# Kernel tuning notes

Measured on AMD Instinct MI355X. Metric: run time of the kernel, lower is better.

## Reference

```python
import jax, jax.numpy as jnp
import numpy as np
from functools import partial

IMG = 800
ANCHOR_SIZES = (32.0, 64.0, 128.0, 256.0, 512.0)
RATIOS = (0.5, 1.0, 2.0)
PRE_NMS = 1000
POST_NMS = 1000
NMS_TH = 0.7
MIN_SIZE = 1e-3
POOL = 7
SRATIO = 2  # roi_align sampling_ratio
SCALES = (0.25, 0.125, 0.0625, 0.03125)
BBOX_CLIP = float(np.log(1000.0 / 16.0))


def _cell_anchors(size):
    r = jnp.asarray(RATIOS, jnp.float32)
    hr = jnp.sqrt(r)
    wr = 1.0 / hr
    ws = size * wr
    hs = size * hr
    return jnp.round(jnp.stack([-ws / 2, -hs / 2, ws / 2, hs / 2], axis=1))  # [A,4]


def _grid_anchors(gh, gw, sh, sw, cell):
    sx = jnp.arange(gw, dtype=jnp.float32) * sw
    sy = jnp.arange(gh, dtype=jnp.float32) * sh
    yy, xx = jnp.meshgrid(sy, sx, indexing='ij')
    shifts = jnp.stack([xx, yy, xx, yy], axis=-1).reshape(-1, 4)
    # order: H-major, W, then A anchors per cell (matches torchvision)
    return (shifts[:, None, :] + cell[None, :, :]).reshape(-1, 4)


def _flatten_level(obj, dl):
    # permute_and_flatten: [B,A,H,W] -> [B,H*W*A], [B,4A,H,W] -> [B,H*W*A,4]
    B, A, H, W = obj.shape
    o = obj.transpose(0, 2, 3, 1).reshape(B, -1)
    d = dl.reshape(B, A, 4, H, W).transpose(0, 3, 4, 1, 2).reshape(B, -1, 4)
    return o, d


def _decode(deltas, anchors):
    # BoxCoder.decode with weights (1,1,1,1)
    w = anchors[:, 2] - anchors[:, 0]
    h = anchors[:, 3] - anchors[:, 1]
    cx = anchors[:, 0] + 0.5 * w
    cy = anchors[:, 1] + 0.5 * h
    dx, dy = deltas[..., 0], deltas[..., 1]
    dw = jnp.minimum(deltas[..., 2], BBOX_CLIP)
    dh = jnp.minimum(deltas[..., 3], BBOX_CLIP)
    pcx = dx * w + cx
    pcy = dy * h + cy
    pw = jnp.exp(dw) * w
    ph = jnp.exp(dh) * h
    return jnp.stack([pcx - 0.5 * pw, pcy - 0.5 * ph, pcx + 0.5 * pw, pcy + 0.5 * ph], axis=-1)


def _iou_one(box, boxes):
    a1 = (box[2] - box[0]) * (box[3] - box[1])
    a2 = (boxes[:, 2] - boxes[:, 0]) * (boxes[:, 3] - boxes[:, 1])
    lt = jnp.maximum(box[:2], boxes[:, :2])
    rb = jnp.minimum(box[2:], boxes[:, 2:])
    wh = jnp.clip(rb - lt, 0.0)
    inter = wh[:, 0] * wh[:, 1]
    return inter / (a1 + a2 - inter)


def _nms(boxes, scores, k):
    # greedy NMS, fixed k iterations (jit-friendly)
    def step(s, _):
        i = jnp.argmax(s)
        sup = _iou_one(boxes[i], boxes) > NMS_TH
        s = jnp.where(sup, -jnp.inf, s).at[i].set(-jnp.inf)
        return s, i
    _, idx = jax.lax.scan(step, scores, None, length=k)
    return idx


def _roi_align(feat, rois, scale):
    # feat [C,H,W], rois [R,4] in image coords -> [R,C,POOL,POOL]; aligned=False semantics
    C, H, W = feat.shape
    R = rois.shape[0]
    x1, y1 = rois[:, 0] * scale, rois[:, 1] * scale
    x2, y2 = rois[:, 2] * scale, rois[:, 3] * scale
    rw = jnp.maximum(x2 - x1, 1.0)
    rh = jnp.maximum(y2 - y1, 1.0)
    S = POOL * SRATIO
    t = (jnp.arange(S, dtype=jnp.float32) + 0.5) / S
    y = jnp.broadcast_to((y1[:, None] + rh[:, None] * t)[:, :, None], (R, S, S))
    x = jnp.broadcast_to((x1[:, None] + rw[:, None] * t)[:, None, :], (R, S, S))
    mask = (y >= -1.0) & (y <= H) & (x >= -1.0) & (x <= W)
    yc = jnp.clip(y, 0.0, H - 1.0)
    xc = jnp.clip(x, 0.0, W - 1.0)
    y0 = jnp.floor(yc).astype(jnp.int32)
    x0 = jnp.floor(xc).astype(jnp.int32)
    y1i = jnp.minimum(y0 + 1, H - 1)
    x1i = jnp.minimum(x0 + 1, W - 1)
    ly = yc - y0
    lx = xc - x0
    v00 = feat[:, y0, x0]
    v01 = feat[:, y0, x1i]
    v10 = feat[:, y1i, x0]
    v11 = feat[:, y1i, x1i]  # [C,R,S,S]
    val = ((1 - ly) * (1 - lx) * v00 + (1 - ly) * lx * v01 + ly * (1 - lx) * v10 + ly * lx * v11) * mask
    pooled = val.reshape(C, R, POOL, SRATIO, POOL, SRATIO).mean(axis=(3, 5))
    return pooled.transpose(1, 0, 2, 3)


def _forward(image_tensors, feats, objs, dls):
    B = image_tensors.shape[0]
    grids = [o.shape[-2:] for o in objs]
    anchors = jnp.concatenate([
        _grid_anchors(gh, gw, float(IMG // gh), float(IMG // gw), _cell_anchors(s))
        for (gh, gw), s in zip(grids, ANCHOR_SIZES)], axis=0)
    flat = [_flatten_level(o, d) for o, d in zip(objs, dls)]
    # RPN detaches both objectness and deltas before proposal filtering
    obj = jax.lax.stop_gradient(jnp.concatenate([f[0] for f in flat], axis=1))   # [B,N]
    dl = jax.lax.stop_gradient(jnp.concatenate([f[1] for f in flat], axis=1))    # [B,N,4]
    proposals = _decode(dl, anchors)                                             # [B,N,4]
    npl = [3 * gh * gw for gh, gw in grids]
    offs = np.concatenate([[0], np.cumsum(npl)])
    idx_parts, lvl_parts = [], []
    for l, n in enumerate(npl):
        k = min(PRE_NMS, n)
        _, ix = jax.lax.top_k(obj[:, offs[l]:offs[l + 1]], k)
        idx_parts.append(ix + offs[l])
        lvl_parts.append(jnp.full((k,), l, jnp.float32))
    idx = jnp.concatenate(idx_parts, axis=1)   # [B,K]
    lvl = jnp.concatenate(lvl_parts)           # [K]
    boxes = jnp.take_along_axis(proposals, idx[..., None], axis=1)
    scores = jax.nn.sigmoid(jnp.take_along_axis(obj, idx, axis=1))
    boxes = jnp.clip(boxes, 0.0, float(IMG))   # clip_boxes_to_image (square image)
    ws = boxes[..., 2] - boxes[..., 0]
    hs = boxes[..., 3] - boxes[..., 1]
    valid = (ws >= MIN_SIZE) & (hs >= MIN_SIZE)  # remove_small_boxes via score masking
    scores = jnp.where(valid, scores, -jnp.inf)
    # batched_nms: offset boxes per level so NMS is independent across levels
    off_boxes = boxes + (lvl * (IMG + 1.0))[None, :, None]
    keep = jax.vmap(lambda b, s: _nms(b, s, POST_NMS))(off_boxes, scores)  # [B,POST]
    props = jnp.take_along_axis(boxes, keep[..., None], axis=1)            # [B,POST,4]
    # MultiScaleRoIAlign level mapping (k0=4, canonical 224)
    area = (props[..., 2] - props[..., 0]) * (props[..., 3] - props[..., 1])
    li = jnp.clip(jnp.floor(4.0 + jnp.log2(jnp.sqrt(area) / 224.0 + 1e-6)), 2.0, 5.0).astype(jnp.int32) - 2
    R = props.shape[1]
    C = feats[0].shape[1]
    box_feats = jnp.zeros((B, R, C, POOL, POOL), feats[0].dtype)
    for l, (f, sc) in enumerate(zip(feats, SCALES)):
        pooled = jax.vmap(partial(_roi_align, scale=sc))(f, props)  # [B,R,C,7,7]
        box_feats = box_feats + pooled * (li == l)[..., None, None, None]
    return props, box_feats.reshape(B * R, C, POOL, POOL)


def setup_inputs() -> dict:
    key = jax.random.key(0)
    ks = jax.random.split(key, 16)
    B, C = 2, 256
    grids = [(200, 200), (100, 100), (50, 50), (25, 25), (13, 13)]
    d = {}
    d['image_tensors'] = jax.random.normal(ks[0], (B, 3, IMG, IMG), jnp.float32)
    for i in range(4):
        gh, gw = grids[i]
        d[f'features_{i}'] = jax.random.normal(ks[1 + i], (B, C, gh, gw), jnp.float32)
    for i in range(5):
        gh, gw = grids[i]
        d[f'objectness_{i}'] = jax.random.normal(ks[5 + i], (B, 3, gh, gw), jnp.float32)
        d[f'pred_bbox_deltas_{i}'] = jax.random.normal(ks[10 + i], (B, 12, gh, gw), jnp.float32)
    return d


def reference(image_tensors, features_0, features_1, features_2, features_3,
              objectness_0, objectness_1, objectness_2, objectness_3, objectness_4,
              pred_bbox_deltas_0, pred_bbox_deltas_1, pred_bbox_deltas_2,
              pred_bbox_deltas_3, pred_bbox_deltas_4):
    feats = [features_0, features_1, features_2, features_3]
    objs = [objectness_0, objectness_1, objectness_2, objectness_3, objectness_4]
    dls = [pred_bbox_deltas_0, pred_bbox_deltas_1, pred_bbox_deltas_2,
           pred_bbox_deltas_3, pred_bbox_deltas_4]
    return _forward(image_tensors, feats, objs, dls)
```

## Files before the change

kernel.cpp:

```cpp
#include <hip/hip_runtime.h>
#include <math.h>

typedef unsigned int u32;
typedef unsigned long long u64;

#define N_ALL 159882
#define NC 4507
#define MROW 72
#define NEGINF_KEY 0x007FFFFFu
#define IMGF 800.0f
#define BBOX_CLIP_F 4.135166556742356f

#define NHWC_L1 10240000u
#define NHWC_L2 12800000u
#define NHWC_L3 13440000u
#define NHWC_BS 13600000u

__constant__ int   c_offs[5]  = {0,120000,150000,157500,159375};
__constant__ int   c_gw[5]    = {200,100,50,25,13};
__constant__ float c_stride[5]= {4.f,8.f,16.f,32.f,61.f};
__constant__ float c_size[5]  = {32.f,64.f,128.f,256.f,512.f};
__constant__ int   c_koff[5]  = {0,1000,2000,3000,4000};
__constant__ int   c_k[5]     = {1000,1000,1000,1000,507};
__constant__ float c_ratio[3] = {0.5f,1.f,2.f};

struct PtrArgs { const float* obj[5]; const float* dl[5]; };

__device__ __forceinline__ u32 fkey32f(float x){
  u32 u = __float_as_uint(x);
  return (u & 0x80000000u) ? ~u : (u | 0x80000000u);
}
__device__ __forceinline__ int level_of(int g){
  return (g >= 159375) ? 4 : (g >= 157500) ? 3 : (g >= 150000) ? 2 : (g >= 120000) ? 1 : 0;
}
__device__ __forceinline__ u64 readlane64(u64 v, int l){
  u32 lo = (u32)v, hi = (u32)(v >> 32);
  u32 a = (u32)__builtin_amdgcn_readlane((int)lo, l);
  u32 b = (u32)__builtin_amdgcn_readlane((int)hi, l);
  return ((u64)b << 32) | (u64)a;
}

__global__ void k_decode(PtrArgs pa, int B, float* boxes_all, u32* key_all, u32* fkey_all){
#pragma clang fp contract(off)
  int idx = blockIdx.x*blockDim.x + threadIdx.x;
  int total = B*N_ALL;
  if (idx >= total) return;
  int b = idx / N_ALL;
  int g = idx - b*N_ALL;
  int l = level_of(g);
  int n = g - c_offs[l];
  int a = n % 3;
  int pos = n / 3;
  int gw = c_gw[l];
  int wx = pos % gw;
  int hy = pos / gw;
  int plane = gw*gw;
  const float* obj = pa.obj[l];
  const float* dl  = pa.dl[l];
  float logit = obj[(size_t)(b*3 + a)*plane + hy*gw + wx];
  size_t dbase = (size_t)(b*12 + a*4)*plane + (size_t)hy*gw + wx;
  float d0 = dl[dbase];
  float d1 = dl[dbase + (size_t)plane];
  float d2 = dl[dbase + (size_t)2*plane];
  float d3 = dl[dbase + (size_t)3*plane];
  float ratio = c_ratio[a];
  float hr = sqrtf(ratio);
  float wr = 1.0f/hr;
  float wsz = c_size[l]*wr;
  float hsz = c_size[l]*hr;
  float ca0 = rintf(-0.5f*wsz), ca1 = rintf(-0.5f*hsz);
  float ca2 = rintf( 0.5f*wsz), ca3 = rintf( 0.5f*hsz);
  float st = c_stride[l];
  float shx = (float)wx*st, shy = (float)hy*st;
  float ax1 = shx+ca0, ay1 = shy+ca1, ax2 = shx+ca2, ay2 = shy+ca3;
  float w = ax2-ax1, h = ay2-ay1;
  float cx = ax1 + 0.5f*w, cy = ay1 + 0.5f*h;
  float dw = fminf(d2, BBOX_CLIP_F), dh = fminf(d3, BBOX_CLIP_F);
  float pcx = d0*w + cx, pcy = d1*h + cy;
  float pw = expf(dw)*w, ph = expf(dh)*h;
  float x1 = pcx - 0.5f*pw, y1 = pcy - 0.5f*ph;
  float x2 = pcx + 0.5f*pw, y2 = pcy + 0.5f*ph;
  x1 = fminf(fmaxf(x1,0.f),IMGF); y1 = fminf(fmaxf(y1,0.f),IMGF);
  x2 = fminf(fmaxf(x2,0.f),IMGF); y2 = fminf(fmaxf(y2,0.f),IMGF);
  bool valid = ((x2-x1) >= 0.001f) && ((y2-y1) >= 0.001f);
  ((float4*)boxes_all)[idx] = make_float4(x1,y1,x2,y2);
  key_all[idx] = fkey32f(logit);
  float sgf = 1.0f/(1.0f + expf(-logit));
  fkey_all[idx] = valid ? fkey32f(sgf) : NEGINF_KEY;
}

__global__ __launch_bounds__(1024) void k_topk(const u32* key_all, u32* cand_g, int B){
  int blk = blockIdx.x;
  int b = blk / 5, l = blk - b*5;
  int g0 = c_offs[l];
  int N  = ((l==4)?N_ALL:c_offs[l+1]) - g0;
  int k  = c_k[l];
  const u32* keys = key_all + (size_t)b*N_ALL + g0;
  u32* out = cand_g + (size_t)b*NC + c_koff[l];
  __shared__ u32 hist[4096];
  __shared__ u64 buf[4096];
  __shared__ int s_bstar, s_chi, s_scnt, s_bcnt;
  int tid = threadIdx.x;
  for (int i=tid;i<4096;i+=1024) hist[i]=0;
  if (tid==0){ s_scnt=0; s_bcnt=0; }
  __syncthreads();
  for (int i=tid;i<N;i+=1024) atomicAdd(&hist[keys[i]>>20], 1u);
  __syncthreads();
  for (int s=1;s<4096;s<<=1){
    u32 v[4];
    for (int j=0;j<4;j++){ int i=tid+j*1024; v[j]=hist[i] + ((i+s<4096)?hist[i+s]:0); }
    __syncthreads();
    for (int j=0;j<4;j++){ int i=tid+j*1024; hist[i]=v[j]; }
    __syncthreads();
  }
  for (int j=0;j<4;j++){
    int i = tid + j*1024;
    u32 suf = hist[i];
    u32 nxt = (i+1<4096)?hist[i+1]:0u;
    if (suf >= (u32)k && nxt < (u32)k){ s_bstar = i; s_chi = (int)nxt; }
  }
  __syncthreads();
  int bstar = s_bstar, chi = s_chi;
  int r = k - chi;
  for (int i=tid;i<N;i+=1024){
    u32 kk = keys[i];
    int bin = (int)(kk>>20);
    if (bin > bstar){
      int slot = atomicAdd(&s_scnt,1);
      out[slot] = (u32)(g0 + i);
    } else if (bin == bstar){
      int slot = atomicAdd(&s_bcnt,1);
      if (slot < 4096) buf[slot] = ((u64)kk<<32) | (u32)(~(u32)(g0+i));
    }
  }
  __syncthreads();
  int m = s_bcnt; if (m > 4096) m = 4096;
  int P = 1; while (P < m) P <<= 1; if (P < 2) P = 2;
  for (int i=m+tid;i<P;i+=1024) buf[i]=0;
  __syncthreads();
  for (u32 ksz=2;ksz<=(u32)P;ksz<<=1){
    for (u32 j=ksz>>1;j>0;j>>=1){
      for (int i=tid;i<P;i+=1024){
        u32 ixj = (u32)i ^ j;
        if (ixj > (u32)i){
          u64 x = buf[i], y = buf[ixj];
          bool up = ((i & ksz) == 0);
          if (up ? (x < y) : (x > y)){ buf[i]=y; buf[ixj]=x; }
        }
      }
      __syncthreads();
    }
  }
  for (int t=tid; t<r && t<m; t+=1024) out[chi + t] = ~(u32)buf[t];
}

__global__ __launch_bounds__(1024) void k_rank(u32* cand_g, const u32* key_all, int B){
  int blk = blockIdx.x; int b = blk/5, l = blk - b*5;
  int k = c_k[l];
  u32* seg = cand_g + (size_t)b*NC + c_koff[l];
  __shared__ u64 sk[1024];
  int tid = threadIdx.x;
  u64 v = 0;
  if (tid < k){
    u32 g = seg[tid];
    v = ((u64)key_all[(size_t)b*N_ALL + g]<<32) | (u32)(~g);
  }
  sk[tid] = v;
  __syncthreads();
  for (u32 ksz=2;ksz<=1024;ksz<<=1){
    for (u32 j=ksz>>1;j>0;j>>=1){
      int i = tid;
      u32 ixj = (u32)i ^ j;
      if (ixj > (u32)i){
        u64 x = sk[i], y = sk[ixj];
        bool up = ((i & ksz) == 0);
        if (up ? (x < y) : (x > y)){ sk[i]=y; sk[ixj]=x; }
      }
      __syncthreads();
    }
  }
  if (tid < k) seg[tid] = ~(u32)sk[tid];
}

__device__ __forceinline__ void merge_elem(const u64* As, const u64* Bs, u64* dst,
                                           int m, int n, int k){
  int lo = k - n; if (lo < 0) lo = 0;
  int hi = (k < m) ? k : m;
  while (lo < hi){
    int mid = (lo + hi) >> 1;
    if (As[mid] > Bs[k-1-mid]) lo = mid + 1; else hi = mid;
  }
  int a = lo, bb = k - lo;
  u64 out;
  if (a < m && (bb >= n || As[a] > Bs[bb])) out = As[a]; else out = Bs[bb];
  dst[k] = out;
}

__global__ __launch_bounds__(1024) void k_sortcand(const u32* cand_g, const u32* fkey_all,
                                                   const float* boxes_all,
                                                   float* sorted_box, float* sorted_off,
                                                   u32* fcnt_ws, float* pos0box){
  __shared__ u64 sA[NC];
  __shared__ u64 sB[NC];
  __shared__ u32 wsum[16];
  __shared__ int s_f;
  int b = blockIdx.x, tid = threadIdx.x;
  int lane = tid & 63, wv = tid >> 6;
  if (tid == 0) s_f = 0;
  size_t cbase = (size_t)b*NC;
  size_t abase = (size_t)b*N_ALL;
  u64 below = lane ? (~0ull >> (64 - lane)) : 0ull;
  for (int l = 0; l < 5; ++l){
    int kl = c_k[l], ko = c_koff[l];
    bool act = tid < kl;
    u32 fk = 0; bool val = false;
    u32 i_g = (u32)(ko + tid);
    if (act){
      u32 g = cand_g[cbase + i_g];
      fk = fkey_all[abase + g];
      val = fk > NEGINF_KEY;
    }
    u64 bal = __ballot(act && val);
    int pv_w = __popcll(bal & below);
    if (lane == 0) wsum[wv] = (u32)__popcll(bal);
    __syncthreads();
    int pre = 0, Vl = 0;
    #pragma unroll
    for (int w2 = 0; w2 < 16; ++w2){
      int s = (int)wsum[w2];
      if (w2 < wv) pre += s;
      Vl += s;
    }
    if (tid == 0) s_f += Vl;
    if (act){
      int pv = pre + pv_w;
      int pos = val ? pv : (Vl + (tid - pv));
      sA[ko + pos] = ((u64)fk << 32) | (u32)(~i_g);
    }
    __syncthreads();
  }
  for (int k = tid; k < NC; k += 1024){
    if (k < 2000)       merge_elem(sA,        sA + 1000, sB,        1000, 1000, k);
    else if (k < 4000)  merge_elem(sA + 2000, sA + 3000, sB + 2000, 1000, 1000, k - 2000);
    else                sB[k] = sA[k];
  }
  __syncthreads();
  for (int k = tid; k < NC; k += 1024){
    if (k < 4000) merge_elem(sB, sB + 2000, sA, 2000, 2000, k);
    else          sA[k] = sB[k];
  }
  __syncthreads();
  for (int k = tid; k < NC; k += 1024){
    merge_elem(sA, sA + 4000, sB, 4000, 507, k);
  }
  __syncthreads();
  for (int i = tid; i < NC; i += 1024){
    u32 posc = ~(u32)sB[i];
    u32 g = cand_g[cbase + posc];
    int lvl = level_of((int)g);
    float4 bx = ((const float4*)boxes_all)[abase + g];
    ((float4*)sorted_box)[cbase + i] = bx;
    float off = 801.0f*(float)lvl;
    ((float4*)sorted_off)[cbase + i] = make_float4(bx.x+off, bx.y+off, bx.z+off, bx.w+off);
  }
  if (tid == 0){
    fcnt_ws[b] = (u32)s_f;
    u32 g0b = cand_g[cbase + 0];
    float4 bx = ((const float4*)boxes_all)[abase + g0b];
    ((float4*)pos0box)[b] = bx;
  }
}

__global__ void k_iou(const float* sorted_off, u64* M){
#pragma clang fp contract(off)
  int i = blockIdx.x, b = blockIdx.y, lane = threadIdx.x;
  const float4* boxes = ((const float4*)sorted_off) + (size_t)b*NC;
  float4 bi = boxes[i];
  float a1 = (bi.z-bi.x)*(bi.w-bi.y);
  u64* row = M + ((size_t)b*NC + i)*MROW;
  for (int w=0; w<71; w++){
    int j = w*64 + lane;
    bool sup = false;
    if (j < NC){
      float4 bj = boxes[j];
      float a2 = (bj.z-bj.x)*(bj.w-bj.y);
      float ltx = fmaxf(bi.x,bj.x), lty = fmaxf(bi.y,bj.y);
      float rbx = fminf(bi.z,bj.z), rby = fminf(bi.w,bj.w);
      float wx = fmaxf(rbx-ltx,0.f), wy = fmaxf(rby-lty,0.f);
      float inter = wx*wy;
      float iou = inter/(a1+a2-inter);
      sup = iou > 0.7f;
    }
    u64 word = __ballot(sup);
    if (lane==0) row[w] = word;
  }
}

#define GETQ2(q) { if (t2){ int jj=__builtin_ctzll(t2); t2&=t2-1; q = &buf[cb][jj*72]; } else q = zbuf; }
__global__ __launch_bounds__(256) void k_nms_tr(const float* sorted_box, const u64* M,
                      const u32* fcnt_ws, const float* pos0box, float* props, int B,
                      const float* f0, const float* f1, const float* f2, const float* f3,
                      float* nhwc, int doTr){
  __shared__ u64 buf[2][64*72];
  __shared__ u64 zbuf[72];
  __shared__ int ki[1000];
  __shared__ int s_kc, s_done;
  int bid = blockIdx.x;
  int tid = threadIdx.x;
  if (bid >= B){
    float (*t)[65] = reinterpret_cast<float(*)[65]>(&buf[0][0]);
    int id = bid - B;
    int b = id / 3328;
    int rem = id - b*3328;
    int P, W; const float* f; u32 loff;
    if (rem < 2500){ W=200; f=f0; loff=0u; }
    else if (rem < 3128){ W=100; f=f1; loff=NHWC_L1; rem -= 2500; }
    else if (rem < 3288){ W=50;  f=f2; loff=NHWC_L2; rem -= 3128; }
    else { W=25; f=f3; loff=NHWC_L3; rem -= 3288; }
    P = W*W;
    int ctile = rem & 3, ptile = rem >> 2;
    int c0 = ctile*64, p0 = ptile*64;
    const float* src = f + (size_t)b*256*P;
    float* dst = nhwc + (size_t)b*NHWC_BS + loff;
    int q   = tid & 15;
    int cl0 = tid >> 4;
    bool vec4ok = ((P & 3) == 0);
    int p = p0 + 4*q;
    float4 v[4];
    #pragma unroll
    for (int k = 0; k < 4; ++k){
      int cl = cl0 + 16*k;
      const float* s = src + (size_t)(c0+cl)*P + p;
      if (vec4ok && (p + 3 < P)){
        v[k] = *(const float4*)s;
      } else {
        v[k].x = (p   < P) ? s[0] : 0.f;
        v[k].y = (p+1 < P) ? s[1] : 0.f;
        v[k].z = (p+2 < P) ? s[2] : 0.f;
        v[k].w = (p+3 < P) ? s[3] : 0.f;
      }
    }
    #pragma unroll
    for (int k = 0; k < 4; ++k){
      int cl = cl0 + 16*k;
      t[cl][4*q+0] = v[k].x; t[cl][4*q+1] = v[k].y;
      t[cl][4*q+2] = v[k].z; t[cl][4*q+3] = v[k].w;
    }
    __syncthreads();
    #pragma unroll
    for (int k = 0; k < 4; ++k){
      int pl = cl0 + 16*k;
      int pp = p0 + pl;
      if (pp < P){
        float4 o = make_float4(t[4*q+0][pl], t[4*q+1][pl],
                               t[4*q+2][pl], t[4*q+3][pl]);
        *(float4*)(dst + (size_t)pp*256 + c0 + 4*q) = o;
      }
    }
    return;
  }
  int b = bid;
  int F = (int)fcnt_ws[b];
  const u64* Mb = M + (size_t)b*NC*MROW;
  int nch = (F + 63) >> 6;
  int lane = tid & 63, wv = tid >> 6;
  if (tid == 0){ s_kc = 0; s_done = (nch == 0) ? 1 : 0; }
  if (tid < 72) zbuf[tid] = 0ull;
  if (nch > 0){
    for (int e = tid; e < 64*72; e += 256){
      int rr = e / 72, wo = e - rr*72;
      int r2 = rr; if (r2 > NC-1) r2 = NC-1;
      buf[0][e] = Mb[(size_t)r2*MROW + wo];
    }
  }
  u64 rg[24];
  if (wv > 0 && nch > 1){
    #pragma unroll
    for (int k = 0; k < 24; ++k){
      int e = (tid - 64) + k*192;
      int rr = e/72, wo = e - rr*72;
      int r2 = 64 + rr; if (r2 > NC-1) r2 = NC-1;
      rg[k] = Mb[(size_t)r2*MROW + wo];
    }
  }
  __syncthreads();
  u64 sup0 = 0, sup1 = 0;
  int kc = 0;
  for (int c = 0; c < nch; ++c){
    int cb = c & 1;
    if (wv > 0){
      if (c + 1 < nch){
        #pragma unroll
        for (int k = 0; k < 24; ++k){
          int e = (tid - 64) + k*192;
          buf[cb^1][e] = rg[k];
        }
      }
      if (c + 2 < nch){
        int base2 = (c + 2) << 6;
        #pragma unroll
        for (int k = 0; k < 24; ++k){
          int e = (tid - 64) + k*192;
          int rr = e/72, wo = e - rr*72;
          int r2 = base2 + rr; if (r2 > NC-1) r2 = NC-1;
          rg[k] = Mb[(size_t)r2*MROW + wo];
        }
      }
    } else if (kc < 1000){
      int base = c << 6;
      int cnt = F - base; if (cnt > 64) cnt = 64;
      u64 supw = (c < 64) ? readlane64(sup0, c) : readlane64(sup1, c - 64);
      u64 alive = ~supw;
      if (cnt < 64) alive &= ((1ull << cnt) - 1ull);
      u64 wrow = buf[cb][lane*72 + c];
      u64 below = lane ? (~0ull >> (64 - lane)) : 0ull;
      u64 colb = wrow & below;
      bool myal = ((alive >> lane) & 1ull) != 0ull;
      u64 kept = __ballot(myal);
      #pragma unroll 1
      for (int it = 0; it < 64; ++it){
        bool kj = myal && ((kept & colb) == 0ull);
        u64 nk = __ballot(kj);
        if (nk == kept) break;
        kept = nk;
      }
      int cnt_k = __popcll(kept);
      int rank  = __popcll(kept & below);
      int budget = 1000 - kc;
      bool sel = ((kept >> lane) & 1ull) && (rank < budget);
      if (sel) ki[kc + rank] = base + lane;
      if (cnt_k >= budget){
        if (lane == 0){ s_done = 1; s_kc = 1000; }
      } else {
        kc += cnt_k;
        u64 t2 = kept;
        while (t2){
          const u64 *q0,*q1,*q2,*q3,*q4,*q5,*q6,*q7;
          const u64 *q8,*q9,*q10,*q11,*q12,*q13,*q14,*q15;
          GETQ2(q0) GETQ2(q1) GETQ2(q2) GETQ2(q3)
          GETQ2(q4) GETQ2(q5) GETQ2(q6) GETQ2(q7)
          GETQ2(q8) GETQ2(q9) GETQ2(q10) GETQ2(q11)
          GETQ2(q12) GETQ2(q13) GETQ2(q14) GETQ2(q15)
          u64 a0=q0[lane],a1=q1[lane],a2=q2[lane],a3=q3[lane];
          u64 a4=q4[lane],a5=q5[lane],a6=q6[lane],a7=q7[lane];
          u64 a8=q8[lane],a9=q9[lane],a10=q10[lane],a11=q11[lane];
          u64 a12=q12[lane],a13=q13[lane],a14=q14[lane],a15=q15[lane];
          sup0 |= (((a0|a1)|(a2|a3))|((a4|a5)|(a6|a7)))
                | (((a8|a9)|(a10|a11))|((a12|a13)|(a14|a15)));
          if (lane < 7){
            u64 b0=q0[64+lane],b1=q1[64+lane],b2=q2[64+lane],b3=q3[64+lane];
            u64 b4=q4[64+lane],b5=q5[64+lane],b6=q6[64+lane],b7=q7[64+lane];
            u64 b8=q8[64+lane],b9=q9[64+lane],b10=q10[64+lane],b11=q11[64+lane];
            u64 b12=q12[64+lane],b13=q13[64+lane],b14=q14[64+lane],b15=q15[64+lane];
            sup1 |= (((b0|b1)|(b2|b3))|((b4|b5)|(b6|b7)))
                  | (((b8|b9)|(b10|b11))|((b12|b13)|(b14|b15)));
          }
        }
        if (lane == 0) s_kc = kc;
      }
    }
    __syncthreads();
    if (s_done) break;
  }
  __syncthreads();
  int kcf = s_kc;
  const float* sb = sorted_box + (size_t)b*NC*4;
  float* pb = props + (size_t)b*4000;
  float4 p0v = ((const float4*)pos0box)[b];
  float pv[4] = {p0v.x, p0v.y, p0v.z, p0v.w};
  for (int idx = tid; idx < 4000; idx += 256){
    int k4 = idx >> 2, comp = idx & 3;
    float v = (k4 < kcf) ? sb[(size_t)ki[k4]*4 + comp] : pv[comp];
    pb[idx] = v;
  }
}

__global__ __launch_bounds__(256) void k_roi_nhwc(const float* nhwc, const float* props,
                                                  float* out){
#pragma clang fp contract(off)
  int r = blockIdx.x;
  int b = r / 1000;
  int tid = threadIdx.x;
  __shared__ float s_ly[14], s_lx[14], s_ym[14], s_xm[14];
  __shared__ int   s_y0[14], s_y1[14], s_x0[14], s_x1[14];
  __shared__ float obuf[49*257];
  float bx0 = props[(size_t)r*4+0], by0 = props[(size_t)r*4+1];
  float bx1 = props[(size_t)r*4+2], by1 = props[(size_t)r*4+3];
  float area = (bx1-bx0)*(by1-by0);
  float v = 4.0f + log2f(sqrtf(area)/224.0f + 1e-6f);
  float fl = floorf(v);
  fl = fminf(fmaxf(fl, 2.0f), 5.0f);
  int li = (int)fl - 2;
  int H = (li==0)?200:(li==1)?100:(li==2)?50:25;
  u32 loff = (li==0)?0u:(li==1)?NHWC_L1:(li==2)?NHWC_L2:NHWC_L3;
  float scale = (li==0)?0.25f:(li==1)?0.125f:(li==2)?0.0625f:0.03125f;
  float x1 = bx0*scale, y1 = by0*scale, x2 = bx1*scale, y2 = by1*scale;
  float rw = fmaxf(x2-x1, 1.0f), rh = fmaxf(y2-y1, 1.0f);
  if (tid < 14){
    float t = ((float)tid + 0.5f)/14.0f;
    float yv = y1 + rh*t;
    s_ym[tid] = (yv >= -1.0f && yv <= (float)H) ? 1.0f : 0.0f;
    float yc = fminf(fmaxf(yv,0.0f),(float)(H-1));
    int iy0 = (int)floorf(yc);
    s_y0[tid]=iy0; s_y1[tid]=min(iy0+1,H-1); s_ly[tid]=yc-(float)iy0;
    float xv = x1 + rw*t;
    s_xm[tid] = (xv >= -1.0f && xv <= (float)H) ? 1.0f : 0.0f;
    float xc = fminf(fmaxf(xv,0.0f),(float)(H-1));
    int ix0 = (int)floorf(xc);
    s_x0[tid]=ix0; s_x1[tid]=min(ix0+1,H-1); s_lx[tid]=xc-(float)ix0;
  }
  __syncthreads();
  const float* src = nhwc + (size_t)b*NHWC_BS + loff;
  float* orow = out + (size_t)r*12544;
  for (int py = 0; py < 7; ++py){
    for (int px = 0; px < 7; ++px){
      float sum = 0.f;
      #pragma unroll
      for (int iy = 0; iy < 2; ++iy){
        int syi = py*2+iy;
        int yy0 = s_y0[syi], yy1 = s_y1[syi];
        float ly = s_ly[syi], fy = s_ym[syi];
        #pragma unroll
        for (int ix = 0; ix < 2; ++ix){
          int sxi = px*2+ix;
          int xx0 = s_x0[sxi], xx1 = s_x1[sxi];
          float lx = s_lx[sxi], fx = s_xm[sxi];
          const float* p00 = src + ((size_t)yy0*H + xx0)*256;
          const float* p01 = src + ((size_t)yy0*H + xx1)*256;
          const float* p10 = src + ((size_t)yy1*H + xx0)*256;
          const float* p11 = src + ((size_t)yy1*H + xx1)*256;
          float v00 = p00[tid], v01 = p01[tid], v10 = p10[tid], v11 = p11[tid];
          float val = ((1.f-ly)*(1.f-lx)*v00 + (1.f-ly)*lx*v01
                     + ly*(1.f-lx)*v10 + ly*lx*v11) * (fy*fx);
          sum += val;
        }
      }
      obuf[(py*7+px)*257 + tid] = sum*0.25f;
    }
  }
  __syncthreads();
  for (int o = tid; o < 12544; o += 256){
    int c = o/49, p = o - c*49;
    orow[o] = obuf[p*257 + c];
  }
}

__global__ __launch_bounds__(256) void k_roi(const float* f0, const float* f1,
                                             const float* f2, const float* f3,
                                             const float* props, float* out){
#pragma clang fp contract(off)
  int r = blockIdx.x;
  int b = r / 1000;
  int tid = threadIdx.x;
  __shared__ float s_ly[14], s_lx[14], s_ym[14], s_xm[14];
  __shared__ int   s_y0[14], s_y1[14], s_x0[14], s_x1[14];
  float bx0 = props[(size_t)r*4+0], by0 = props[(size_t)r*4+1];
  float bx1 = props[(size_t)r*4+2], by1 = props[(size_t)r*4+3];
  float area = (bx1-bx0)*(by1-by0);
  float v = 4.0f + log2f(sqrtf(area)/224.0f + 1e-6f);
  float fl = floorf(v);
  fl = fminf(fmaxf(fl, 2.0f), 5.0f);
  int li = (int)fl - 2;
  const float* fptr = (li==0)?f0:(li==1)?f1:(li==2)?f2:f3;
  int H = (li==0)?200:(li==1)?100:(li==2)?50:25;
  float scale = (li==0)?0.25f:(li==1)?0.125f:(li==2)?0.0625f:0.03125f;
  float x1 = bx0*scale, y1 = by0*scale, x2 = bx1*scale, y2 = by1*scale;
  float rw = fmaxf(x2-x1, 1.0f), rh = fmaxf(y2-y1, 1.0f);
  if (tid < 14){
    float t = ((float)tid + 0.5f)/14.0f;
    float yv = y1 + rh*t;
    s_ym[tid] = (yv >= -1.0f && yv <= (float)H) ? 1.0f : 0.0f;
    float yc = fminf(fmaxf(yv,0.0f),(float)(H-1));
    int iy0 = (int)floorf(yc);
    s_y0[tid]=iy0; s_y1[tid]=min(iy0+1,H-1); s_ly[tid]=yc-(float)iy0;
    float xv = x1 + rw*t;
    s_xm[tid] = (xv >= -1.0f && xv <= (float)H) ? 1.0f : 0.0f;
    float xc = fminf(fmaxf(xv,0.0f),(float)(H-1));
    int ix0 = (int)floorf(xc);
    s_x0[tid]=ix0; s_x1[tid]=min(ix0+1,H-1); s_lx[tid]=xc-(float)ix0;
  }
  __syncthreads();
  size_t plane = (size_t)H*H;
  const float* fb = fptr + (size_t)b*256*plane;
  float* orow = out + (size_t)r*12544;
  for (int o=tid; o<12544; o+=256){
    int c = o/49;
    int p = o - c*49;
    int py = p/7, px = p - py*7;
    const float* fc = fb + (size_t)c*plane;
    float sum = 0.f;
    for (int iy=0; iy<2; iy++){
      int syi = py*2+iy;
      int yy0 = s_y0[syi], yy1 = s_y1[syi];
      float ly = s_ly[syi], fy = s_ym[syi];
      for (int ix=0; ix<2; ix++){
        int sxi = px*2+ix;
        int xx0 = s_x0[sxi], xx1 = s_x1[sxi];
        float lx = s_lx[sxi], fx = s_xm[sxi];
        float v00 = fc[yy0*H+xx0], v01 = fc[yy0*H+xx1];
        float v10 = fc[yy1*H+xx0], v11 = fc[yy1*H+xx1];
        float val = ((1.f-ly)*(1.f-lx)*v00 + (1.f-ly)*lx*v01
                   + ly*(1.f-lx)*v10 + ly*lx*v11) * (fy*fx);
        sum += val;
      }
    }
    orow[o] = sum*0.25f;
  }
}

extern "C" void kernel_launch(void* const* d_in, const int* in_sizes, int n_in,
                              void* d_out, int out_size, void* d_ws, size_t ws_size,
                              hipStream_t stream) {
  int B = in_sizes[0] / (3*800*800);
  PtrArgs pa;
  bool interleaved = (n_in >= 7) && (in_sizes[6] == 4*in_sizes[5]);
  for (int i=0;i<5;i++){
    if (interleaved){
      pa.obj[i] = (const float*)d_in[5+2*i];
      pa.dl[i]  = (const float*)d_in[6+2*i];
    } else {
      pa.obj[i] = (const float*)d_in[5+i];
      pa.dl[i]  = (const float*)d_in[10+i];
    }
  }

  auto align256 = [](size_t x){ return (x + 255) & ~(size_t)255; };
  size_t sz_M      = align256(((size_t)B*NC + 1)*MROW*8);
  size_t sz_boxes  = align256((size_t)B*N_ALL*16);
  size_t sz_key    = align256((size_t)B*N_ALL*4);
  size_t sz_fkey   = align256((size_t)B*N_ALL*4);
  size_t sz_cand   = align256((size_t)B*NC*4);
  size_t sz_sbox   = align256((size_t)B*NC*16);
  size_t sz_soff   = align256((size_t)B*NC*16);
  size_t sz_fcnt   = align256((size_t)B*4);
  size_t sz_p0     = align256((size_t)B*16);
  size_t need = sz_M+sz_boxes+sz_key+sz_fkey+sz_cand+sz_sbox+sz_soff+sz_fcnt+sz_p0;
  size_t outBytes = (size_t)out_size * 4;
  size_t start = (outBytes - need) & ~(size_t)255;
  char* w = (char*)d_out + start;
  auto alloc = [&](size_t bytes)->char*{ char* p = w; w += bytes; return p; };

  u64*  M          = (u64*) alloc(sz_M);
  float* boxes_all = (float*)alloc(sz_boxes);
  u32*  key_all    = (u32*) alloc(sz_key);
  u32*  fkey_all   = (u32*) alloc(sz_fkey);
  u32*  cand_g     = (u32*) alloc(sz_cand);
  float* sorted_box= (float*)alloc(sz_sbox);
  float* sorted_off= (float*)alloc(sz_soff);
  u32*  fcnt       = (u32*) alloc(sz_fcnt);
  float* pos0box   = (float*)alloc(sz_p0);

  float* props     = (float*)d_out;
  float* feats_out = (float*)d_out + (size_t)B*1000*4;

  int total = B*N_ALL;
  k_decode<<<(total+255)/256, 256, 0, stream>>>(pa, B, boxes_all, key_all, fkey_all);
  k_topk<<<B*5, 1024, 0, stream>>>(key_all, cand_g, B);
  k_rank<<<B*5, 1024, 0, stream>>>(cand_g, key_all, B);
  k_sortcand<<<B, 1024, 0, stream>>>(cand_g, fkey_all, boxes_all, sorted_box, sorted_off, fcnt, pos0box);
  k_iou<<<dim3(NC, B), 64, 0, stream>>>(sorted_off, M);

  size_t nhwcBytes = (size_t)B * NHWC_BS * 4;
  int doTr = (ws_size >= nhwcBytes) ? 1 : 0;
  float* nhwc = (float*)d_ws;
  int grid = B + (doTr ? B*3328 : 0);
  k_nms_tr<<<grid, 256, 0, stream>>>(sorted_box, M, fcnt, pos0box, props, B,
                                     (const float*)d_in[1], (const float*)d_in[2],
                                     (const float*)d_in[3], (const float*)d_in[4],
                                     nhwc, doTr);
  if (doTr){
    k_roi_nhwc<<<B*1000, 256, 0, stream>>>(nhwc, props, feats_out);
  } else {
    k_roi<<<B*1000, 256, 0, stream>>>((const float*)d_in[1], (const float*)d_in[2],
                                      (const float*)d_in[3], (const float*)d_in[4],
                                      props, feats_out);
  }
}
```

Baseline: 335.5 us.

## Vectorize NHWC RoIAlign gathers with float4 per lane and split bins across wavefronts

The RoIAlign NHWC kernel now precomputes per-sample corner offsets and bilinear weights for all 196 sample points in shared memory. Each wavefront handles a subset of the 49 output bins, and each lane loads four channels with float4 gathers instead of one scalar per thread. This cuts the number of load instructions and the per-thread serial loop over all bins. The cost is extra shared-memory tables and a different floating-point summation order, which may change rounding slightly despite contract(off). The obuf writes from the 4*lane pattern can also cause shared-memory bank conflicts.

```diff
diff --git a/kernel.cpp b/kernel.cpp
--- a/kernel.cpp
+++ b/kernel.cpp
@@ -481,8 +481,9 @@
   int r = blockIdx.x;
   int b = r / 1000;
   int tid = threadIdx.x;
-  __shared__ float s_ly[14], s_lx[14], s_ym[14], s_xm[14];
-  __shared__ int   s_y0[14], s_y1[14], s_x0[14], s_x1[14];
+  int lane = tid & 63, wv = tid >> 6;
+  __shared__ int   s_o0[196], s_o1[196], s_o2[196], s_o3[196];
+  __shared__ float s_a0[196], s_a1[196], s_a2[196], s_a3[196], s_m[196];
   __shared__ float obuf[49*257];
   float bx0 = props[(size_t)r*4+0], by0 = props[(size_t)r*4+1];
   float bx1 = props[(size_t)r*4+2], by1 = props[(size_t)r*4+3];
@@ -496,49 +497,63 @@
   float scale = (li==0)?0.25f:(li==1)?0.125f:(li==2)?0.0625f:0.03125f;
   float x1 = bx0*scale, y1 = by0*scale, x2 = bx1*scale, y2 = by1*scale;
   float rw = fmaxf(x2-x1, 1.0f), rh = fmaxf(y2-y1, 1.0f);
-  if (tid < 14){
-    float t = ((float)tid + 0.5f)/14.0f;
-    float yv = y1 + rh*t;
-    s_ym[tid] = (yv >= -1.0f && yv <= (float)H) ? 1.0f : 0.0f;
+  if (tid < 196){
+    int syi = tid / 14, sxi = tid - syi*14;
+    float ty = ((float)syi + 0.5f)/14.0f;
+    float yv = y1 + rh*ty;
+    float fy = (yv >= -1.0f && yv <= (float)H) ? 1.0f : 0.0f;
     float yc = fminf(fmaxf(yv,0.0f),(float)(H-1));
     int iy0 = (int)floorf(yc);
-    s_y0[tid]=iy0; s_y1[tid]=min(iy0+1,H-1); s_ly[tid]=yc-(float)iy0;
-    float xv = x1 + rw*t;
-    s_xm[tid] = (xv >= -1.0f && xv <= (float)H) ? 1.0f : 0.0f;
+    int iy1 = min(iy0+1,H-1);
+    float ly = yc-(float)iy0;
+    float tx = ((float)sxi + 0.5f)/14.0f;
+    float xv = x1 + rw*tx;
+    float fx = (xv >= -1.0f && xv <= (float)H) ? 1.0f : 0.0f;
     float xc = fminf(fmaxf(xv,0.0f),(float)(H-1));
     int ix0 = (int)floorf(xc);
-    s_x0[tid]=ix0; s_x1[tid]=min(ix0+1,H-1); s_lx[tid]=xc-(float)ix0;
-  }
-  __syncthreads();
-  const float* src = nhwc + (size_t)b*NHWC_BS + loff;
+    int ix1 = min(ix0+1,H-1);
+    float lx = xc-(float)ix0;
+    s_o0[tid] = (iy0*H + ix0)*64;
+    s_o1[tid] = (iy0*H + ix1)*64;
+    s_o2[tid] = (iy1*H + ix0)*64;
+    s_o3[tid] = (iy1*H + ix1)*64;
+    s_a0[tid] = (1.f-ly)*(1.f-lx);
+    s_a1[tid] = (1.f-ly)*lx;
+    s_a2[tid] = ly*(1.f-lx);
+    s_a3[tid] = ly*lx;
+    s_m[tid]  = fy*fx;
+  }
+  __syncthreads();
+  const float4* src4 = (const float4*)(nhwc + (size_t)b*NHWC_BS + loff);
+  for (int p = wv; p < 49; p += 4){
+    int py = p/7, px = p - py*7;
+    float accx = 0.f, accy = 0.f, accz = 0.f, accw = 0.f;
+    #pragma unroll
+    for (int iy = 0; iy < 2; ++iy){
+      #pragma unroll
+      for (int ix = 0; ix < 2; ++ix){
+        int sp = (py*2+iy)*14 + (px*2+ix);
+        int o00 = s_o0[sp], o01 = s_o1[sp], o10 = s_o2[sp], o11 = s_o3[sp];
+        float a00 = s_a0[sp], a01 = s_a1[sp], a10 = s_a2[sp], a11 = s_a3[sp];
+        float m = s_m[sp];
+        float4 v00 = src4[o00 + lane];
+        float4 v01 = src4[o01 + lane];
+        float4 v10 = src4[o10 + lane];
+        float4 v11 = src4[o11 + lane];
+        accx += (a00*v00.x + a01*v01.x + a10*v10.x + a11*v11.x)*m;
+        accy += (a00*v00.y + a01*v01.y + a10*v10.y + a11*v11.y)*m;
+        accz += (a00*v00.z + a01*v01.z + a10*v10.z + a11*v11.z)*m;
+        accw += (a00*v00.w + a01*v01.w + a10*v10.w + a11*v11.w)*m;
+      }
+    }
+    int ob = p*257 + 4*lane;
+    obuf[ob+0] = accx*0.25f;
+    obuf[ob+1] = accy*0.25f;
+    obuf[ob+2] = accz*0.25f;
+    obuf[ob+3] = accw*0.25f;
+  }
+  __syncthreads();
   float* orow = out + (size_t)r*12544;
-  for (int py = 0; py < 7; ++py){
-    for (int px = 0; px < 7; ++px){
-      float sum = 0.f;
-      #pragma unroll
-      for (int iy = 0; iy < 2; ++iy){
-        int syi = py*2+iy;
-        int yy0 = s_y0[syi], yy1 = s_y1[syi];
-        float ly = s_ly[syi], fy = s_ym[syi];
-        #pragma unroll
-        for (int ix = 0; ix < 2; ++ix){
-          int sxi = px*2+ix;
-          int xx0 = s_x0[sxi], xx1 = s_x1[sxi];
-          float lx = s_lx[sxi], fx = s_xm[sxi];
-          const float* p00 = src + ((size_t)yy0*H + xx0)*256;
-          const float* p01 = src + ((size_t)yy0*H + xx1)*256;
-          const float* p10 = src + ((size_t)yy1*H + xx0)*256;
-          const float* p11 = src + ((size_t)yy1*H + xx1)*256;
-          float v00 = p00[tid], v01 = p01[tid], v10 = p10[tid], v11 = p11[tid];
-          float val = ((1.f-ly)*(1.f-lx)*v00 + (1.f-ly)*lx*v01
-                     + ly*(1.f-lx)*v10 + ly*lx*v11) * (fy*fx);
-          sum += val;
-        }
-      }
-      obuf[(py*7+px)*257 + tid] = sum*0.25f;
-    }
-  }
-  __syncthreads();
   for (int o = tid; o < 12544; o += 256){
     int c = o/49, p = o - c*49;
     orow[o] = obuf[p*257 + c];
```

Result: faster. 316.3 us (-5.7%).
